# Performance work log

Measured on AMD Instinct MI355X. Metric: run time of the kernel, lower is better.

The kernel has to match this reference:

```python
import jax, jax.numpy as jnp
import numpy as np

B, T, E = 4, 2048, 2048
G, QG, D = 4, 4, 128  # kv groups, queries per group, head dim; H = G*QG = 16


def rope(x):
    # x: (..., T, D); rotate-half rotary positional embedding over the T axis
    t, d = x.shape[-2], x.shape[-1]
    half = d // 2
    inv_freq = 1.0 / (10000.0 ** (jnp.arange(half, dtype=jnp.float32) / half))
    ang = jnp.arange(t, dtype=jnp.float32)[:, None] * inv_freq[None, :]  # (T, half)
    cos, sin = jnp.cos(ang), jnp.sin(ang)
    x1, x2 = x[..., :half], x[..., half:]
    return jnp.concatenate([x1 * cos - x2 * sin, x1 * sin + x2 * cos], axis=-1)


def setup_inputs() -> dict:
    key = jax.random.key(0)
    ks = jax.random.split(key, 5)
    s = 0.02
    return {
        "x": jax.random.normal(ks[0], (B, T, E), dtype=jnp.float32),
        "Wq": jax.random.normal(ks[1], (E, G * QG * D), dtype=jnp.float32) * s,
        "Wk": jax.random.normal(ks[2], (E, G * D), dtype=jnp.float32) * s,
        "Wv": jax.random.normal(ks[3], (E, G * D), dtype=jnp.float32) * s,
        "Wo": jax.random.normal(ks[4], (G * QG * D, E), dtype=jnp.float32) * s,
    }


def reference(x, Wq, Wk, Wv, Wo):
    b, t, e = x.shape
    q = (x @ Wq).reshape(b, t, G, QG, D).transpose(0, 2, 3, 1, 4)  # (B,G,QG,T,D)
    k = (x @ Wk).reshape(b, t, G, D).transpose(0, 2, 1, 3)          # (B,G,T,D)
    v = (x @ Wv).reshape(b, t, G, D).transpose(0, 2, 1, 3)          # (B,G,T,D)
    q = rope(q)
    k = rope(k)
    scores = jnp.einsum("bgqtd,bgsd->bgqts", q, k) / jnp.sqrt(jnp.float32(D))
    causal = jnp.tril(jnp.ones((t, t), dtype=bool))                 # query t attends to s<=t
    scores = jnp.where(causal, scores, jnp.float32(-1e9))
    probs = jax.nn.softmax(scores, axis=-1)                         # (B,G,QG,T,T) explicit probs
    attn = jnp.einsum("bgqts,bgsd->bgqtd", probs, v)
    out = attn.transpose(0, 3, 1, 2, 4).reshape(b, t, G * QG * D)
    return out @ Wo
```

## Files before the change

### kernel.cpp

```cpp
#include <hip/hip_runtime.h>
#include <hip/hip_bf16.h>

typedef unsigned short u16;
typedef unsigned u32;
typedef float f32x4 __attribute__((ext_vector_type(4)));
typedef float f32x16 __attribute__((ext_vector_type(16)));
typedef short bf16x8 __attribute__((ext_vector_type(8)));

#define B_ 4
#define T_ 2048
#define E_ 2048
#define G_ 4
#define QG_ 4
#define D_ 128
#define H_ 16
#define BT_ 8192
#define SCALE2 0.12752745907f

__device__ __forceinline__ u16 f2bf(float f) {
  union { float f; unsigned u; } v; v.f = f;
  unsigned r = v.u + 0x7fffu + ((v.u >> 16) & 1u);
  return (u16)(r >> 16);
}
__device__ __forceinline__ float bf2f(u16 b) {
  union { unsigned u; float f; } v; v.u = ((unsigned)b) << 16;
  return v.f;
}
__device__ __forceinline__ unsigned packbf2(float lo, float hi) {
  __hip_bfloat162 h2 = __float22bfloat162_rn(make_float2(lo, hi));
  union { __hip_bfloat162 h; unsigned u; } cv; cv.h = h2; return cv.u;
}
#define EXP2F(x) __builtin_amdgcn_exp2f(x)

#define GL2LDS(g, l) __builtin_amdgcn_global_load_lds( \
    (const __attribute__((address_space(1))) void*)(g), \
    (__attribute__((address_space(3))) void*)(l), 16, 0, 0)

#define MFMA(a, b, c) __builtin_amdgcn_mfma_f32_16x16x32_bf16((a), (b), (c), 0, 0, 0)
#define MFMA32(a, b, c) __builtin_amdgcn_mfma_f32_32x32x16_bf16((a), (b), (c), 0, 0, 0)


__global__ void k_cvt_x(const float4* __restrict__ x, uint2* __restrict__ xb) {
  int i = blockIdx.x * 256 + threadIdx.x;
  float4 v = x[i];
  uint2 o;
  o.x = (unsigned)f2bf(v.x) | ((unsigned)f2bf(v.y) << 16);
  o.y = (unsigned)f2bf(v.z) | ((unsigned)f2bf(v.w) << 16);
  xb[i] = o;
}

__global__ void k_cvt_wT(const float* __restrict__ W, u16* __restrict__ WT,
                         int R, int C) {
  __shared__ float tile[64][65];
  int c0 = blockIdx.x * 64, r0 = blockIdx.y * 64;
  int tid = threadIdx.x;
#pragma unroll
  for (int p = 0; p < 16; ++p) {
    int idx = p * 256 + tid;
    int i = idx >> 6, j = idx & 63;
    tile[i][j] = W[(size_t)(r0 + i) * C + c0 + j];
  }
  __syncthreads();
#pragma unroll
  for (int p = 0; p < 16; ++p) {
    int idx = p * 256 + tid;
    int i = idx >> 6, j = idx & 63;
    WT[(size_t)(c0 + i) * R + r0 + j] = f2bf(tile[j][i]);
  }
}

__global__ void k_tables(float* __restrict__ ct, float* __restrict__ st) {
  int i = blockIdx.x * 256 + threadIdx.x;
  int t = i >> 6, j = i & 63;
  float freq = powf(10000.f, -(float)j / 64.f);
  float ang = (float)t * freq;
  ct[i] = cosf(ang);
  st[i] = sinf(ang);
}


__device__ __forceinline__ void rd_frag(bf16x8* dst, const u16* Xs,
                                        int r0, int r1, int r2, int r3,
                                        int lo, int hi) {
  int rows[4] = {r0, r1, r2, r3};
#pragma unroll
  for (int i = 0; i < 4; ++i) {
    int rw = rows[i] + lo;
    dst[i] = *(const bf16x8*)&Xs[(rw >> 1) * 64 +
        (((((rw & 1) << 2) | hi)) ^ ((rw >> 1) & 7)) * 8];
  }
}
__device__ __forceinline__ void mm16(f32x4 (*acc)[4], const bf16x8* a,
                                     const bf16x8* b) {
#pragma unroll
  for (int i = 0; i < 4; ++i)
#pragma unroll
    for (int j = 0; j < 4; ++j)
      acc[i][j] = MFMA(a[i], b[j], acc[i][j]);
}

template <int MODE>
__global__ __launch_bounds__(512, 2) void k_gemm256(
    const u16* __restrict__ A, const u16* __restrict__ Bt,
    void* __restrict__ C, const float* __restrict__ ct,
    const float* __restrict__ st, u16* __restrict__ kout,
    u16* __restrict__ vout, int M, int N, int K) {
  __shared__ u16 As[4][8192];
  __shared__ u16 Bs[4][8192];
  const int tid = threadIdx.x;
  const int wave = tid >> 6, lane = tid & 63;
  const int lo = lane & 15, hi = lane >> 4;
  const int nbn = N >> 8;
  const int bn = blockIdx.x % nbn;
  const int bm = blockIdx.x / nbn;
  const int m0 = bm * 256, n0 = bn * 256;
  const int wm = wave >> 2, wn = wave & 3;
  const int bbase = (MODE == 3) ? ((wn & 1) * 32 + (wn >> 1) * 128) : wn * 64;
  const int BO2 = (MODE == 3) ? 64 : 32;
  const int BO3 = (MODE == 3) ? 80 : 48;

  f32x4 acc[8][4] = {};

  auto stage = [&](const u16* __restrict__ X, int x0, u16* dstBase, int kcol) {
#pragma unroll
    for (int r = 0; r < 2; ++r) {
      int idx = r * 512 + tid;
      int pair = idx >> 3;
      int u = (idx & 7) ^ (pair & 7);
      GL2LDS(X + (size_t)(x0 + pair * 2 + (u >> 2)) * K + kcol + (u & 3) * 8,
             dstBase + (r * 512 + wave * 64) * 8);
    }
  };

  const int NT = K >> 6;
  stage(A, m0, &As[0][0], 0);
  stage(Bt, n0, &Bs[0][0], 0);
  stage(A, m0, &As[1][0], 32);
  stage(Bt, n0, &Bs[1][0], 32);
  asm volatile("s_waitcnt vmcnt(4)" ::: "memory");
  __builtin_amdgcn_s_barrier();

  for (int t = 0; t < NT; ++t) {
    const int s0 = (t & 1) << 1;
    const int sn = s0 ^ 2;
    const bool pf = (t + 1 < NT);
    const int kc = (t + 1) << 6;

    bf16x8 b0[4], b1[4], a[4];
    rd_frag(b0, &Bs[s0][0], bbase, bbase + 16, bbase + BO2, bbase + BO3, lo, hi);
    rd_frag(a, &As[s0][0], wm * 128, wm * 128 + 16, wm * 128 + 32, wm * 128 + 48, lo, hi);
    if (pf) stage(A, m0, &As[sn][0], kc);
    __builtin_amdgcn_s_barrier();
    __builtin_amdgcn_s_setprio(1);
    mm16(&acc[0], a, b0);
    __builtin_amdgcn_s_setprio(0);
    __builtin_amdgcn_s_barrier();
    rd_frag(a, &As[s0][0], wm * 128 + 64, wm * 128 + 80, wm * 128 + 96, wm * 128 + 112, lo, hi);
    if (pf) {
      stage(Bt, n0, &Bs[sn][0], kc);
      asm volatile("s_waitcnt vmcnt(4)" ::: "memory");
    } else {
      asm volatile("s_waitcnt vmcnt(0)" ::: "memory");
    }
    __builtin_amdgcn_s_barrier();
    __builtin_amdgcn_s_setprio(1);
    mm16(&acc[4], a, b0);
    __builtin_amdgcn_s_setprio(0);
    __builtin_amdgcn_s_barrier();
    rd_frag(b1, &Bs[s0 + 1][0], bbase, bbase + 16, bbase + BO2, bbase + BO3, lo, hi);
    rd_frag(a, &As[s0 + 1][0], wm * 128, wm * 128 + 16, wm * 128 + 32, wm * 128 + 48, lo, hi);
    if (pf) stage(A, m0, &As[sn + 1][0], kc + 32);
    __builtin_amdgcn_s_barrier();
    __builtin_amdgcn_s_setprio(1);
    mm16(&acc[0], a, b1);
    __builtin_amdgcn_s_setprio(0);
    __builtin_amdgcn_s_barrier();
    rd_frag(a, &As[s0 + 1][0], wm * 128 + 64, wm * 128 + 80, wm * 128 + 96, wm * 128 + 112, lo, hi);
    if (pf) {
      stage(Bt, n0, &Bs[sn + 1][0], kc + 32);
      asm volatile("s_waitcnt vmcnt(4)" ::: "memory");
    }
    __builtin_amdgcn_s_barrier();
    __builtin_amdgcn_s_setprio(1);
    mm16(&acc[4], a, b1);
    __builtin_amdgcn_s_setprio(0);
    __builtin_amdgcn_s_barrier();
  }

  if (MODE == 3) {
    if (bn >= 10) {
      const int n0v = n0 - 2560;
#pragma unroll
      for (int i = 0; i < 8; ++i)
#pragma unroll
        for (int j = 0; j < 4; ++j)
#pragma unroll
          for (int r = 0; r < 4; ++r) {
            int row = m0 + wm * 128 + i * 16 + hi * 4 + r;
            int col = n0v + bbase + (j & 1) * 16 + (j >> 1) * 64 + lo;
            vout[(size_t)row * 512 + col] = f2bf(acc[i][j][r]);
          }
    } else {
      const bool isq = (bn < 8);
      u16* out = isq ? (u16*)C : kout;
      const int hh = (isq ? (n0 >> 7) : ((n0 - 2048) >> 7)) + (wn >> 1);
      const int hbits = isq ? 4 : 2;
      const float sc = isq ? SCALE2 : 1.0f;
#pragma unroll
      for (int i = 0; i < 8; ++i)
#pragma unroll
        for (int r = 0; r < 4; ++r) {
          int rr = m0 + wm * 128 + i * 16 + hi * 4 + r;
          int bb = rr >> 11, tt = rr & (T_ - 1);
          size_t ro = ((size_t)((bb << hbits) + hh) * T_ + tt) << 7;
#pragma unroll
          for (int j = 0; j < 2; ++j) {
            int d1 = (wn & 1) * 32 + j * 16 + lo;
            float c = ct[tt * 64 + d1], s = st[tt * 64 + d1];
            float x1 = acc[i][j][r], x2 = acc[i][j + 2][r];
            out[ro + d1]      = f2bf((x1 * c - x2 * s) * sc);
            out[ro + d1 + 64] = f2bf((x1 * s + x2 * c) * sc);
          }
        }
    }
  } else {
#pragma unroll
    for (int i = 0; i < 8; ++i)
#pragma unroll
      for (int j = 0; j < 4; ++j)
#pragma unroll
        for (int r = 0; r < 4; ++r) {
          int row = m0 + wm * 128 + i * 16 + hi * 4 + r;
          int col = n0 + wn * 64 + j * 16 + lo;
          ((float*)C)[(size_t)row * N + col] = acc[i][j][r];
        }
  }
}

__global__ void k_vtrans(const u16* __restrict__ vg, u16* __restrict__ vT,
                         int sstr) {
  __shared__ u16 tile[64][65];
  int t0 = blockIdx.x * 64;
  int d0 = blockIdx.y * 64;
  int bg = blockIdx.z;
  int g = bg & (G_ - 1), b = bg >> 2;
  int tid = threadIdx.x;
#pragma unroll
  for (int p = 0; p < 16; ++p) {
    int idx = p * 256 + tid;
    int i = idx >> 6, j = idx & 63;
    tile[i][j] = vg[(size_t)(b * T_ + t0 + i) * sstr + g * D_ + d0 + j];
  }
  __syncthreads();
#pragma unroll
  for (int p = 0; p < 16; ++p) {
    int idx = p * 256 + tid;
    int i = idx >> 6, j = idx & 63;
    vT[((size_t)bg * D_ + d0 + i) * T_ + t0 + j] = tile[j][i];
  }
}


__device__ __forceinline__ void swap32(u32 a, u32 b, u32& x, u32& y) {
#if __has_builtin(__builtin_amdgcn_permlane32_swap)
  auto rr = __builtin_amdgcn_permlane32_swap(a, b, false, false);
  x = rr[0]; y = rr[1];
#else
  u32 as = __shfl_xor(a, 32), bs = __shfl_xor(b, 32);
  int hi = (threadIdx.x & 63) >> 5;
  x = hi ? bs : a;
  y = hi ? b : as;
#endif
}

__global__ __launch_bounds__(256, 2) void k_attn(
    const u16* __restrict__ qh, const u16* __restrict__ kh,
    const u16* __restrict__ vT, u16* __restrict__ ab) {
  __shared__ u16 Ks[2][64 * 128];
  __shared__ u16 Vs[2][128 * 64];
  const int tid = threadIdx.x;
  const int wave = tid >> 6;
  const int lane = tid & 63;
  const int l5 = lane & 31, h1 = lane >> 5;

  const int f = blockIdx.x;
  const int xcd = f & 7;
  const int slot = f >> 3;
  const int bg = xcd * 2 + (slot & 1);
  const int rest = slot >> 1;
  const int qg = rest & 3;
  const int i0 = (15 - (rest >> 2)) * 128;
  const int b = bg >> 2, g = bg & 3;
  const int h = g * 4 + qg;
  const int bh = b * 16 + h;

  const int qw0 = i0 + wave * 32;
  const int q = qw0 + l5;

  const u16* Qrow = qh + ((size_t)bh * T_ + q) * D_;
  bf16x8 qf[8];
#pragma unroll
  for (int kk = 0; kk < 8; ++kk)
    qf[kk] = *(const bf16x8*)(Qrow + kk * 16 + h1 * 8);

  const u16* Kbase = kh + (size_t)(b * G_ + g) * T_ * D_;
  const u16* Vbase = vT + (size_t)(b * G_ + g) * D_ * T_;

  auto stage = [&](int bi, int s0) {
#pragma unroll
    for (int r = 0; r < 4; ++r) {
      int p = r * 256 + tid;
      {
        int row = p >> 4, c = p & 15;
        GL2LDS(Kbase + (size_t)(s0 + row) * D_ + ((c ^ (row & 7)) * 8),
               &Ks[bi][(r * 256 + wave * 64) * 8]);
      }
      {
        int row = p >> 3, c = p & 7;
        GL2LDS(Vbase + (size_t)row * T_ + s0 + ((c ^ (row & 7)) * 8),
               &Vs[bi][(r * 256 + wave * 64) * 8]);
      }
    }
  };

  f32x16 acc[4] = {};
  float mrun = -1e30f, lrun = 0.f;

  const int nt = ((i0 + 127) >> 6) + 1;
  stage(0, 0);
  int bufc = 0;
  for (int ti = 0; ti < nt; ++ti) {
    const int s0 = ti << 6;
    __syncthreads();
    if (ti + 1 < nt) stage(bufc ^ 1, (ti + 1) << 6);
    if (s0 <= qw0 + 31) {
      f32x16 sa[2] = {};
#pragma unroll
      for (int st = 0; st < 2; ++st) {
        if (s0 + st * 32 <= qw0 + 31) {
#pragma unroll
          for (int kk = 0; kk < 8; ++kk) {
            int row = st * 32 + l5;
            bf16x8 kf = *(const bf16x8*)
                &Ks[bufc][row * 128 + ((2 * kk + h1) ^ (row & 7)) * 8];
            sa[st] = MFMA32(kf, qf[kk], sa[st]);
          }
        }
      }
#pragma unroll
      for (int st = 0; st < 2; ++st) {
        const bool needm = (s0 + st * 32 + 31 > qw0);
        if (needm) {
#pragma unroll
          for (int r = 0; r < 16; ++r) {
            int s = s0 + st * 32 + (r & 3) + 8 * (r >> 2) + 4 * h1;
            if (s > q) sa[st][r] = -1e9f;
          }
        }
      }
      float mx[16];
#pragma unroll
      for (int r = 0; r < 16; ++r) mx[r] = fmaxf(sa[0][r], sa[1][r]);
#pragma unroll
      for (int off = 8; off >= 1; off >>= 1)
#pragma unroll
        for (int r = 0; r < 8; ++r)
          if (r < off) mx[r] = fmaxf(mx[r], mx[r + off]);
      float pm = fmaxf(mx[0], __shfl_xor(mx[0], 32));
      if (!__all(pm - mrun <= 8.f)) {
        float mn = fmaxf(mrun, pm);
        float alpha = EXP2F(mrun - mn);
#pragma unroll
        for (int dt = 0; dt < 4; ++dt)
#pragma unroll
          for (int r = 0; r < 16; ++r) acc[dt][r] *= alpha;
        lrun *= alpha;
        mrun = mn;
      }
      bf16x8 pf[4];
      float se[16];
#pragma unroll
      for (int st = 0; st < 2; ++st) {
        float pe[16];
#pragma unroll
        for (int r = 0; r < 16; ++r) {
          pe[r] = EXP2F(sa[st][r] - mrun);
          if (st == 0) se[r] = pe[r]; else se[r] += pe[r];
        }
#pragma unroll
        for (int kl = 0; kl < 2; ++kl) {
          u32 w0 = packbf2(pe[kl * 8 + 0], pe[kl * 8 + 1]);
          u32 w1 = packbf2(pe[kl * 8 + 2], pe[kl * 8 + 3]);
          u32 y0 = packbf2(pe[kl * 8 + 4], pe[kl * 8 + 5]);
          u32 y1 = packbf2(pe[kl * 8 + 6], pe[kl * 8 + 7]);
          union { u32 w[4]; bf16x8 v; } pw;
          swap32(w0, y0, pw.w[0], pw.w[2]);
          swap32(w1, y1, pw.w[1], pw.w[3]);
          pf[st * 2 + kl] = pw.v;
        }
      }
#pragma unroll
      for (int off = 8; off >= 1; off >>= 1)
#pragma unroll
        for (int r = 0; r < 8; ++r)
          if (r < off) se[r] += se[r + off];
      lrun += se[0] + __shfl_xor(se[0], 32);
#pragma unroll
      for (int ks = 0; ks < 4; ++ks) {
#pragma unroll
        for (int dt = 0; dt < 4; ++dt) {
          int row = dt * 32 + l5;
          bf16x8 vf = *(const bf16x8*)
              &Vs[bufc][row * 64 + ((2 * ks + h1) ^ (row & 7)) * 8];
          acc[dt] = MFMA32(vf, pf[ks], acc[dt]);
        }
      }
    }
    bufc ^= 1;
  }
  const float iv = 1.f / lrun;
  u16* outrow = ab + ((size_t)(b * T_ + q)) * (H_ * D_) + (size_t)h * D_;
#pragma unroll
  for (int dt = 0; dt < 4; ++dt)
#pragma unroll
    for (int g4 = 0; g4 < 4; ++g4) {
      uint2 o;
      o.x = (u32)f2bf(acc[dt][g4 * 4 + 0] * iv) |
            ((u32)f2bf(acc[dt][g4 * 4 + 1] * iv) << 16);
      o.y = (u32)f2bf(acc[dt][g4 * 4 + 2] * iv) |
            ((u32)f2bf(acc[dt][g4 * 4 + 3] * iv) << 16);
      *(uint2*)(outrow + dt * 32 + 8 * g4 + 4 * h1) = o;
    }
}


extern "C" void kernel_launch(void* const* d_in, const int* in_sizes, int n_in,
                              void* d_out, int out_size, void* d_ws, size_t ws_size,
                              hipStream_t stream) {
  const float* x  = (const float*)d_in[0];
  const float* Wq = (const float*)d_in[1];
  const float* Wk = (const float*)d_in[2];
  const float* Wv = (const float*)d_in[3];
  const float* Wo = (const float*)d_in[4];

  char* base = (char*)d_ws;
  size_t off = 0;
  auto nxt = [&](size_t bytes) {
    char* r = base + off;
    off += (bytes + 255) & ~(size_t)255;
    return r;
  };
  u16*   xb   = (u16*)nxt((size_t)BT_ * E_ * 2);
  u16*   wAll = (u16*)nxt((size_t)3072 * E_ * 2);
  u16*   woT  = (u16*)nxt((size_t)E_ * E_ * 2);
  float* ct   = (float*)nxt((size_t)T_ * 64 * 4);
  float* st   = (float*)nxt((size_t)T_ * 64 * 4);
  u16*   qhb  = (u16*)nxt((size_t)BT_ * E_ * 2);
  u16*   khb  = (u16*)nxt((size_t)BT_ * (G_ * D_) * 2);
  u16*   vg   = (u16*)nxt((size_t)BT_ * (G_ * D_) * 2);
  u16*   vTb  = (u16*)nxt((size_t)BT_ * (G_ * D_) * 2);
  u16* ab = xb;

  k_cvt_x<<<BT_ * E_ / 4 / 256, 256, 0, stream>>>((const float4*)x, (uint2*)xb);
  k_cvt_wT<<<dim3(E_ / 64, E_ / 64), 256, 0, stream>>>(Wq, wAll, E_, E_);
  k_cvt_wT<<<dim3((G_ * D_) / 64, E_ / 64), 256, 0, stream>>>(
      Wk, wAll + (size_t)2048 * E_, E_, G_ * D_);
  k_cvt_wT<<<dim3((G_ * D_) / 64, E_ / 64), 256, 0, stream>>>(
      Wv, wAll + (size_t)2560 * E_, E_, G_ * D_);
  k_cvt_wT<<<dim3(E_ / 64, E_ / 64), 256, 0, stream>>>(Wo, woT, E_, E_);
  k_tables<<<T_ * 64 / 256, 256, 0, stream>>>(ct, st);

  k_gemm256<3><<<dim3((3072 / 256) * (BT_ / 256)), 512, 0, stream>>>(
      xb, wAll, qhb, ct, st, khb, vg, BT_, 3072, E_);

  k_vtrans<<<dim3(T_ / 64, D_ / 64, B_ * G_), 256, 0, stream>>>(vg, vTb, 512);

  k_attn<<<dim3(1024), 256, 0, stream>>>(qhb, khb, vTb, ab);

  k_gemm256<0><<<dim3((E_ / 256) * (BT_ / 256)), 512, 0, stream>>>(
      ab, woT, d_out, nullptr, nullptr, nullptr, nullptr, BT_, E_, E_);
}
```

Before: 326.5 us.

## Stage K/V in MFMA-fragment-major LDS layout and coalesce GEMM fp32 stores via LDS

The attention kernel now loads K and V tiles into shared memory so that each MFMA operand fragment is a contiguous 512-element block. Each lane then reads its fragment with a simple lane*8 offset, which drops the XOR-swizzle address arithmetic and should avoid bank conflicts. Separately, the fp32 GEMM epilogue stages each 16x64 accumulator slice in LDS and writes it out as row-contiguous float4 stores instead of scattered scalar stores. This reuses the As buffer and adds waitcnt barriers, which relies on that buffer being free after the main loop.

```diff
diff --git a/kernel.cpp b/kernel.cpp
--- a/kernel.cpp
+++ b/kernel.cpp
@@ -224,16 +224,26 @@
         }
     }
   } else {
-#pragma unroll
-    for (int i = 0; i < 8; ++i)
+    float* tb = (float*)&As[0][0] + wave * 1024;
+    const int row0 = m0 + wm * 128;
+    const int col0 = n0 + wn * 64;
+#pragma unroll
+    for (int i = 0; i < 8; ++i) {
 #pragma unroll
       for (int j = 0; j < 4; ++j)
 #pragma unroll
-        for (int r = 0; r < 4; ++r) {
-          int row = m0 + wm * 128 + i * 16 + hi * 4 + r;
-          int col = n0 + wn * 64 + j * 16 + lo;
-          ((float*)C)[(size_t)row * N + col] = acc[i][j][r];
-        }
+        for (int r = 0; r < 4; ++r)
+          tb[(hi * 4 + r) * 64 + j * 16 + lo] = acc[i][j][r];
+      asm volatile("s_waitcnt lgkmcnt(0)" ::: "memory");
+#pragma unroll
+      for (int c4 = 0; c4 < 4; ++c4) {
+        int idx = c4 * 64 + lane;
+        int rr = idx >> 4, cb = (idx & 15) * 4;
+        float4 v = *(float4*)&tb[rr * 64 + cb];
+        *(float4*)&((float*)C)[(size_t)(row0 + i * 16 + rr) * N + col0 + cb] = v;
+      }
+      asm volatile("s_waitcnt lgkmcnt(0)" ::: "memory");
+    }
   }
 }
 
@@ -276,12 +286,13 @@
 __global__ __launch_bounds__(256, 2) void k_attn(
     const u16* __restrict__ qh, const u16* __restrict__ kh,
     const u16* __restrict__ vT, u16* __restrict__ ab) {
-  __shared__ u16 Ks[2][64 * 128];
-  __shared__ u16 Vs[2][128 * 64];
+  __shared__ u16 Ks[2][16 * 512];
+  __shared__ u16 Vs[2][16 * 512];
   const int tid = threadIdx.x;
   const int wave = tid >> 6;
   const int lane = tid & 63;
   const int l5 = lane & 31, h1 = lane >> 5;
+  const int lane8 = lane * 8;
 
   const int f = blockIdx.x;
   const int xcd = f & 7;
@@ -309,17 +320,13 @@
   auto stage = [&](int bi, int s0) {
 #pragma unroll
     for (int r = 0; r < 4; ++r) {
-      int p = r * 256 + tid;
-      {
-        int row = p >> 4, c = p & 15;
-        GL2LDS(Kbase + (size_t)(s0 + row) * D_ + ((c ^ (row & 7)) * 8),
-               &Ks[bi][(r * 256 + wave * 64) * 8]);
-      }
-      {
-        int row = p >> 3, c = p & 7;
-        GL2LDS(Vbase + (size_t)row * T_ + s0 + ((c ^ (row & 7)) * 8),
-               &Vs[bi][(r * 256 + wave * 64) * 8]);
-      }
+      int u = r * 4 + wave;
+      GL2LDS(Kbase + (size_t)(s0 + (u >> 3) * 32 + l5) * D_ +
+                 (u & 7) * 16 + h1 * 8,
+             &Ks[bi][(r * 256 + wave * 64) * 8]);
+      GL2LDS(Vbase + (size_t)((u & 3) * 32 + l5) * T_ + s0 +
+                 (u >> 2) * 16 + h1 * 8,
+             &Vs[bi][(r * 256 + wave * 64) * 8]);
     }
   };
 
@@ -340,9 +347,7 @@
         if (s0 + st * 32 <= qw0 + 31) {
 #pragma unroll
           for (int kk = 0; kk < 8; ++kk) {
-            int row = st * 32 + l5;
-            bf16x8 kf = *(const bf16x8*)
-                &Ks[bufc][row * 128 + ((2 * kk + h1) ^ (row & 7)) * 8];
+            bf16x8 kf = *(const bf16x8*)&Ks[bufc][(st * 8 + kk) * 512 + lane8];
             sa[st] = MFMA32(kf, qf[kk], sa[st]);
           }
         }
@@ -409,9 +414,7 @@
       for (int ks = 0; ks < 4; ++ks) {
 #pragma unroll
         for (int dt = 0; dt < 4; ++dt) {
-          int row = dt * 32 + l5;
-          bf16x8 vf = *(const bf16x8*)
-              &Vs[bufc][row * 64 + ((2 * ks + h1) ^ (row & 7)) * 8];
+          bf16x8 vf = *(const bf16x8*)&Vs[bufc][(ks * 4 + dt) * 512 + lane8];
           acc[dt] = MFMA32(vf, pf[ks], acc[dt]);
         }
       }
```

Measured after the change: 348.4 us. +6.7%, slower.
